# Kernel optimization log

Hardware: AMD Instinct MI355X
Metric: run time of the kernel (lower is better)

The kernel has to match this reference:

```python
import jax, jax.numpy as jnp
import numpy as np

N = 100_000      # nodes
E = 1_600_000    # edges
D = 128          # dim_in == dim_h
L = 3            # num_layers
G = 512          # num graphs in batch
EPS = 1e-5       # BatchNorm1d eps


def setup_inputs() -> dict:
    key = jax.random.key(0)
    k1, k2, k3, k4 = jax.random.split(key, 4)
    x = jax.random.normal(k1, (N, D), dtype=jnp.float32)
    edge_index = jax.random.randint(k2, (2, E), 0, N, dtype=jnp.int64)
    batch = jnp.sort(jax.random.randint(k3, (N,), 0, G, dtype=jnp.int64))
    Ws = jax.random.normal(k4, (L, D, D), dtype=jnp.float32) * 0.05
    bs = jnp.zeros((L, D), dtype=jnp.float32)
    gammas = jnp.ones((L, D), dtype=jnp.float32)
    betas = jnp.zeros((L, D), dtype=jnp.float32)
    return {"x": x, "edge_index": edge_index, "batch": batch,
            "Ws": Ws, "bs": bs, "gammas": gammas, "betas": betas}


def reference(x, edge_index, batch, Ws, bs, gammas, betas):
    src, dst = edge_index[0], edge_index[1]
    # GCN symmetric normalization with self-loops (PyG GCNConv default):
    # deg counts incoming edges at dst, +1 for the self-loop.
    deg = jnp.zeros((N,), dtype=x.dtype).at[dst].add(1.0) + 1.0
    inv_sqrt = jax.lax.rsqrt(deg)
    edge_coeff = inv_sqrt[src] * inv_sqrt[dst]   # [E]
    self_coeff = inv_sqrt * inv_sqrt             # [N] self-loop weight deg^-1

    h = x
    for i in range(L):
        hw = h @ Ws[i]                                           # [N, D]
        agg = (jnp.zeros_like(hw).at[dst].add(hw[src] * edge_coeff[:, None])
               + hw * self_coeff[:, None] + bs[i])               # [N, D]
        # BatchNorm1d (training-mode batch statistics, biased variance)
        mean = agg.mean(axis=0)
        var = agg.var(axis=0)
        hn = (agg - mean) * jax.lax.rsqrt(var + EPS) * gammas[i] + betas[i]
        h = jax.nn.relu(hn)

    # global_add_pool: scatter-add node features by graph id
    return jax.ops.segment_sum(h, batch, num_segments=G)        # [G, D]
```

## Files before the change

kernel.cpp:

```cpp
#include <hip/hip_runtime.h>

#define D 128
#define CHUNK 512
#define NSLICE 8
#define SLW 16

using short8 = __attribute__((ext_vector_type(8))) short;
using f32x4  = __attribute__((ext_vector_type(4))) float;
using f32x2  = __attribute__((ext_vector_type(2))) float;

__device__ __forceinline__ unsigned short f2bf(float f){
  unsigned u = __builtin_bit_cast(unsigned, f);
  u += 0x7fffu + ((u >> 16) & 1u);
  return (unsigned short)(u >> 16);
}
__device__ __forceinline__ float bflo2f(unsigned v){
  return __builtin_bit_cast(float, v << 16);
}
__device__ __forceinline__ float bfhi2f(unsigned v){
  return __builtin_bit_cast(float, v & 0xffff0000u);
}
__device__ __forceinline__ float bfs2f(unsigned short v){
  return __builtin_bit_cast(float, ((unsigned)v) << 16);
}
__device__ __forceinline__ unsigned cvtpk(float lo, float hi){
  unsigned r;
  asm("v_cvt_pk_bf16_f32 %0, %1, %2" : "=v"(r) : "v"(lo), "v"(hi));
  return r;
}

__global__ void k_deg(const int* __restrict__ dst, int* __restrict__ deg, int E){
  int e = blockIdx.x * 256 + threadIdx.x;
  if (e < E) atomicAdd(&deg[dst[e]], 1);
}

__global__ void k_chunksum(const int* __restrict__ deg, int* __restrict__ csum, int n){
  __shared__ int s[256];
  int tid = threadIdx.x;
  int n0 = blockIdx.x * CHUNK + tid * 2;
  int v = 0;
  if (n0     < n) v += deg[n0];
  if (n0 + 1 < n) v += deg[n0 + 1];
  s[tid] = v; __syncthreads();
  for (int off = 128; off > 0; off >>= 1){
    if (tid < off) s[tid] += s[tid + off];
    __syncthreads();
  }
  if (tid == 0) csum[blockIdx.x] = s[0];
}

__global__ void k_scanchunks(int* __restrict__ csum, int nchunks){
  __shared__ int s[256];
  int tid = threadIdx.x;
  int v = (tid < nchunks) ? csum[tid] : 0;
  s[tid] = v; __syncthreads();
  for (int off = 1; off < 256; off <<= 1){
    int t = (tid >= off) ? s[tid - off] : 0;
    __syncthreads();
    s[tid] += t;
    __syncthreads();
  }
  if (tid < nchunks) csum[tid] = s[tid] - v;
}

__global__ void k_offsets(const int* __restrict__ deg, const int* __restrict__ csum,
                          int* __restrict__ offs, float* __restrict__ inv, int n){
  __shared__ int s[256];
  int tid = threadIdx.x;
  int n0 = blockIdx.x * CHUNK + tid * 2;
  int d0 = (n0     < n) ? deg[n0]     : 0;
  int d1 = (n0 + 1 < n) ? deg[n0 + 1] : 0;
  int pair = d0 + d1;
  s[tid] = pair; __syncthreads();
  for (int off = 1; off < 256; off <<= 1){
    int t = (tid >= off) ? s[tid - off] : 0;
    __syncthreads();
    s[tid] += t;
    __syncthreads();
  }
  int excl = s[tid] - pair + csum[blockIdx.x];
  if (n0     <= n) offs[n0]     = excl;
  if (n0 + 1 <= n) offs[n0 + 1] = excl + d0;
  if (n0     < n) inv[n0]     = rsqrtf((float)(d0 + 1));
  if (n0 + 1 < n) inv[n0 + 1] = rsqrtf((float)(d1 + 1));
}

__global__ __launch_bounds__(256)
void k_csrfill(const int* __restrict__ src, const int* __restrict__ dst,
               const int* __restrict__ offs, int* __restrict__ cursor,
               int* __restrict__ csrc, int E, int n){
  int part = blockIdx.x & 7;
  int blk  = blockIdx.x >> 3;
  int nblk = gridDim.x >> 3;
  int per = (n + 7) / 8;
  int d0 = part * per, d1 = min(d0 + per, n);
  int stride = nblk * 256;
  for (int e = blk * 256 + threadIdx.x; e < E; e += stride){
    int d = dst[e];
    if (d >= d0 && d < d1){
      int s = src[e];
      int pos = offs[d] + atomicAdd(&cursor[d], 1);
      csrc[pos] = s;
    }
  }
}

#define WSTRIDE 136
__global__ __launch_bounds__(512)
void k_gemm(const float* __restrict__ hf, const unsigned short* __restrict__ hb,
            const float* __restrict__ W, const float* __restrict__ inv,
            const float* __restrict__ scale, const float* __restrict__ shift,
            int do_norm, unsigned short* __restrict__ hwS, int nrows){
  __shared__ unsigned short Wt[128 * WSTRIDE];
  int tid = threadIdx.x;
  for (int i = tid; i < 128 * 128; i += 512){
    int k = i >> 7, c = i & 127;
    Wt[c * WSTRIDE + k] = f2bf(W[i]);
  }
  __syncthreads();

  int wave = tid >> 6, lane = tid & 63;
  int r0 = blockIdx.x * 128 + wave * 16;
  int row = r0 + (lane & 15);
  int kg = lane >> 4;
  int rowc = row < nrows ? row : nrows - 1;

  short8 a[4];
  if (do_norm){
#pragma unroll
    for (int kt = 0; kt < 4; ++kt){
      int k0 = kt * 32 + kg * 8;
      int sl = k0 >> 4, o = k0 & 15;
      short8 raw = *(const short8*)(hb + ((long)sl * nrows + rowc) * SLW + o);
      unsigned u[4];
#pragma unroll
      for (int j = 0; j < 4; ++j){
        float lo = bfs2f((unsigned short)raw[2*j]);
        float hi = bfs2f((unsigned short)raw[2*j+1]);
        lo = fmaxf(0.f, lo * scale[k0+2*j]   + shift[k0+2*j]);
        hi = fmaxf(0.f, hi * scale[k0+2*j+1] + shift[k0+2*j+1]);
        u[j] = cvtpk(lo, hi);
      }
      a[kt] = *(short8*)u;
    }
  } else {
    const float* hrow = hf + (long)rowc * D;
#pragma unroll
    for (int kt = 0; kt < 4; ++kt){
      int k0 = kt * 32 + kg * 8;
      f32x4 v0 = *(const f32x4*)(hrow + k0);
      f32x4 v1 = *(const f32x4*)(hrow + k0 + 4);
      unsigned u[4];
      u[0] = cvtpk(v0[0], v0[1]);
      u[1] = cvtpk(v0[2], v0[3]);
      u[2] = cvtpk(v1[0], v1[1]);
      u[3] = cvtpk(v1[2], v1[3]);
      a[kt] = *(short8*)u;
    }
  }

  f32x4 acc[8] = {};
#pragma unroll
  for (int ct = 0; ct < 8; ++ct){
    int col = ct * 16 + (lane & 15);
    const unsigned short* bp = &Wt[col * WSTRIDE + kg * 8];
#pragma unroll
    for (int kt = 0; kt < 4; ++kt){
      short8 b = *(const short8*)(bp + kt * 32);
      acc[ct] = __builtin_amdgcn_mfma_f32_16x16x32_bf16(a[kt], b, acc[ct], 0, 0, 0);
    }
  }

  int colbase = lane & 15;
  int rowo = r0 + kg * 4;
  float ivr[4];
#pragma unroll
  for (int r = 0; r < 4; ++r) ivr[r] = inv[min(rowo + r, nrows - 1)];
#pragma unroll
  for (int ct = 0; ct < 8; ++ct){
#pragma unroll
    for (int r = 0; r < 4; ++r){
      int rr = rowo + r;
      if (rr < nrows)
        hwS[((long)ct * nrows + rr) * SLW + colbase] = f2bf(acc[ct][r] * ivr[r]);
    }
  }
}

__global__ __launch_bounds__(256)
void k_agg(const unsigned short* __restrict__ hwS, const float* __restrict__ inv,
           const int* __restrict__ offs, const int* __restrict__ csrc,
           const float* __restrict__ bias,
           unsigned* __restrict__ aggS, float* __restrict__ stats, int n,
           int ngroups){
  int g   = blockIdx.x & 7;
  int grp = blockIdx.x >> 3;
  int tid = threadIdx.x, lane = tid & 63, wv = tid >> 6;
  int ns = lane >> 3;
  int cp = lane & 7;
  int nwaves = ngroups * 4;
  int gw = grp * 4 + wv;
  int per = (n + nwaves - 1) / nwaves;
  int n0 = min(gw * per, n), n1 = min(n0 + per, n);

  const unsigned* slice = (const unsigned*)hwS + (long)g * n * 8;
  unsigned* oslice = aggS + (long)g * n * 8;

  float b0 = bias[g * 16 + cp * 2], b1 = bias[g * 16 + cp * 2 + 1];
  float s0 = 0, s1 = 0, q0 = 0, q1 = 0;

  for (int base = n0; base < n1; base += 8){
    int node = base + ns;
    bool act = node < n1;
    int ndc = act ? node : n1 - 1;
    int e  = offs[ndc];
    int ee = offs[ndc + 1];
    float a0 = 0, a1 = 0;

    int i0 = csrc[(e     < ee) ? e     : 0];
    int i1 = csrc[(e + 1 < ee) ? e + 1 : 0];
    int i2 = csrc[(e + 2 < ee) ? e + 2 : 0];
    int i3 = csrc[(e + 3 < ee) ? e + 3 : 0];
    while (__any(e < ee)){
      int j0 = csrc[(e + 4 < ee) ? e + 4 : 0];
      int j1 = csrc[(e + 5 < ee) ? e + 5 : 0];
      int j2 = csrc[(e + 6 < ee) ? e + 6 : 0];
      int j3 = csrc[(e + 7 < ee) ? e + 7 : 0];
      unsigned v0 = slice[i0 * 8 + cp];
      unsigned v1 = slice[i1 * 8 + cp];
      unsigned v2 = slice[i2 * 8 + cp];
      unsigned v3 = slice[i3 * 8 + cp];
      v0 = (e     < ee) ? v0 : 0u;
      v1 = (e + 1 < ee) ? v1 : 0u;
      v2 = (e + 2 < ee) ? v2 : 0u;
      v3 = (e + 3 < ee) ? v3 : 0u;
      a0 += (bflo2f(v0) + bflo2f(v1)) + (bflo2f(v2) + bflo2f(v3));
      a1 += (bfhi2f(v0) + bfhi2f(v1)) + (bfhi2f(v2) + bfhi2f(v3));
      i0 = j0; i1 = j1; i2 = j2; i3 = j3;
      e += 4;
    }

    if (act){
      unsigned selfv = slice[node * 8 + cp];
      float ivd = inv[node];
      a0 = (a0 + bflo2f(selfv)) * ivd + b0;
      a1 = (a1 + bfhi2f(selfv)) * ivd + b1;
      unsigned pk = ((unsigned)f2bf(a1) << 16) | (unsigned)f2bf(a0);
      __builtin_nontemporal_store(pk, oslice + node * 8 + cp);
      s0 += a0; s1 += a1; q0 += a0 * a0; q1 += a1 * a1;
    }
  }

  s0 += __shfl_xor(s0, 8, 64);  s1 += __shfl_xor(s1, 8, 64);
  q0 += __shfl_xor(q0, 8, 64);  q1 += __shfl_xor(q1, 8, 64);
  s0 += __shfl_xor(s0, 16, 64); s1 += __shfl_xor(s1, 16, 64);
  q0 += __shfl_xor(q0, 16, 64); q1 += __shfl_xor(q1, 16, 64);
  s0 += __shfl_xor(s0, 32, 64); s1 += __shfl_xor(s1, 32, 64);
  q0 += __shfl_xor(q0, 32, 64); q1 += __shfl_xor(q1, 32, 64);

  __shared__ float red[4][8][4];
  if (ns == 0){
    red[wv][cp][0] = s0; red[wv][cp][1] = s1;
    red[wv][cp][2] = q0; red[wv][cp][3] = q1;
  }
  __syncthreads();
  if (tid < 8){
    float t0 = 0, t1 = 0, t2 = 0, t3 = 0;
#pragma unroll
    for (int w = 0; w < 4; ++w){
      t0 += red[w][tid][0]; t1 += red[w][tid][1];
      t2 += red[w][tid][2]; t3 += red[w][tid][3];
    }
    int c = g * 16 + tid * 2;
    atomicAdd(&stats[c],           t0);
    atomicAdd(&stats[c + 1],       t1);
    atomicAdd(&stats[128 + c],     t2);
    atomicAdd(&stats[128 + c + 1], t3);
  }
}

__global__ void k_bn(const float* __restrict__ stats, const float* __restrict__ gamma,
                     const float* __restrict__ beta, float* __restrict__ scale,
                     float* __restrict__ shift, float invn){
  int c = threadIdx.x;
  float mean = stats[c] * invn;
  float var = stats[128 + c] * invn - mean * mean;
  float isd = rsqrtf(var + 1e-5f);
  float sc = gamma[c] * isd;
  scale[c] = sc;
  shift[c] = beta[c] - mean * sc;
}

__global__ __launch_bounds__(256)
void k_pool(const unsigned* __restrict__ aggS, const float* __restrict__ scale,
            const float* __restrict__ shift, const int* __restrict__ batch,
            float* __restrict__ out, int n){
  int tid = threadIdx.x, lane = tid & 63, wv = tid >> 6;
  int gw = blockIdx.x * 4 + wv;
  int n0 = gw * 64;
  if (n0 >= n) return;
  int n1 = min(n0 + 64, n);
  int c0 = lane * 2;
  int sl = lane >> 3, cp = lane & 7;
  long sbase = (long)sl * n * 8;
  float sc0 = scale[c0], sc1 = scale[c0 + 1];
  float sh0 = shift[c0], sh1 = shift[c0 + 1];
  int g = batch[n0];
  float a0 = 0, a1 = 0;
  for (int nd = n0; nd < n1; ++nd){
    int gn = batch[nd];
    if (gn != g){
      atomicAdd(&out[(long)g * D + c0],     a0);
      atomicAdd(&out[(long)g * D + c0 + 1], a1);
      a0 = 0; a1 = 0; g = gn;
    }
    unsigned v = aggS[sbase + (long)nd * 8 + cp];
    a0 += fmaxf(0.f, bflo2f(v) * sc0 + sh0);
    a1 += fmaxf(0.f, bfhi2f(v) * sc1 + sh1);
  }
  atomicAdd(&out[(long)g * D + c0],     a0);
  atomicAdd(&out[(long)g * D + c0 + 1], a1);
}

extern "C" void kernel_launch(void* const* d_in, const int* in_sizes, int n_in,
                              void* d_out, int out_size, void* d_ws, size_t ws_size,
                              hipStream_t stream){
  const float* x      = (const float*)d_in[0];
  const int*   ei     = (const int*)d_in[1];
  const int*   batch  = (const int*)d_in[2];
  const float* Ws     = (const float*)d_in[3];
  const float* bs     = (const float*)d_in[4];
  const float* gammas = (const float*)d_in[5];
  const float* betas  = (const float*)d_in[6];

  const int E_ = in_sizes[1] / 2;
  const int N_ = in_sizes[2];
  const int* src = ei;
  const int* dst = ei + E_;

  char* p = (char*)d_ws;
  auto alloc = [&](size_t bytes) -> void* {
    void* r = (void*)p;
    p += (bytes + 255) & ~(size_t)255;
    return r;
  };
  unsigned*       bufA   = (unsigned*)      alloc((size_t)N_ * D * 2);
  unsigned short* hwS    = (unsigned short*)alloc((size_t)N_ * D * 2);
  int*            deg    = (int*)           alloc((size_t)N_ * 4);
  float*          inv    = (float*)         alloc((size_t)N_ * 4);
  int*            offs   = (int*)           alloc((size_t)(N_ + 1) * 4);
  int*            cursor = (int*)           alloc((size_t)N_ * 4);
  int*            csrc   = (int*)           alloc((size_t)E_ * 4);
  float*          stats  = (float*)         alloc(3 * 256 * 4);
  float*          scales = (float*)         alloc(3 * 128 * 4);
  float*          shifts = (float*)         alloc(3 * 128 * 4);
  int*            csum   = (int*)           alloc(256 * 4);

  hipMemsetAsync(deg,    0, (size_t)N_ * 4, stream);
  hipMemsetAsync(cursor, 0, (size_t)N_ * 4, stream);
  hipMemsetAsync(stats,  0, 3 * 256 * 4, stream);
  hipMemsetAsync(d_out,  0, (size_t)out_size * 4, stream);

  int nchunks = (N_ + CHUNK - 1) / CHUNK;
  k_deg       <<<(E_ + 255) / 256, 256, 0, stream>>>(dst, deg, E_);
  k_chunksum  <<<nchunks, 256, 0, stream>>>(deg, csum, N_);
  k_scanchunks<<<1, 256, 0, stream>>>(csum, nchunks);
  k_offsets   <<<nchunks, 256, 0, stream>>>(deg, csum, offs, inv, N_);
  k_csrfill   <<<2048, 256, 0, stream>>>(src, dst, offs, cursor, csrc, E_, N_);

  int gemm_blocks = (N_ + 127) / 128;
  int ngroups = 256;
  for (int l = 0; l < 3; ++l){
    const float* sc = (l == 0) ? nullptr : scales + (l - 1) * 128;
    const float* sh = (l == 0) ? nullptr : shifts + (l - 1) * 128;
    k_gemm<<<gemm_blocks, 512, 0, stream>>>(x, (const unsigned short*)bufA,
                                            Ws + (size_t)l * D * D, inv, sc, sh,
                                            (l == 0) ? 0 : 1, hwS, N_);
    k_agg<<<ngroups * 8, 256, 0, stream>>>(hwS, inv, offs, csrc, bs + (size_t)l * D,
                                           bufA, stats + (size_t)l * 256, N_, ngroups);
    k_bn<<<1, 128, 0, stream>>>(stats + (size_t)l * 256, gammas + (size_t)l * D,
                                betas + (size_t)l * D, scales + (size_t)l * 128,
                                shifts + (size_t)l * 128, 1.0f / (float)N_);
  }
  k_pool<<<(N_ + 255) / 256, 256, 0, stream>>>(bufA, scales + 2 * 128, shifts + 2 * 128,
                                               batch, (float*)d_out, N_);
}
```

Before: 558.0 us.

## Sort nodes by degree within 64-node windows to balance aggregation waves

Adds a bitonic sort kernel that orders each 64-node window by in-degree, producing a permutation. The aggregation kernel then gives each wave one window, processed as 8 groups of 8 similar-degree nodes, so lanes in a group finish their edge loops together instead of waiting on the slowest node. This also replaces the old launch of 256 groups with one wave per window, creating many more blocks. It costs one extra small sort kernel, an indirect perm load per node, less contiguous output writes, and the nontemporal store is dropped.

```diff
diff --git a/kernel.cpp b/kernel.cpp
--- a/kernel.cpp
+++ b/kernel.cpp
@@ -105,6 +105,30 @@
   }
 }
 
+__global__ __launch_bounds__(256)
+void k_sortwin(const int* __restrict__ deg, int* __restrict__ perm, int n, int W){
+  int wv = threadIdx.x >> 6, lane = threadIdx.x & 63;
+  int win = blockIdx.x * 4 + wv;
+  if (win >= W) return;
+  int idx = win * 64 + lane;
+  int nd2 = idx;
+  int dg  = (idx < n) ? deg[idx] : 0x7fffffff;
+#pragma unroll
+  for (int k = 2; k <= 64; k <<= 1){
+#pragma unroll
+    for (int j = k >> 1; j > 0; j >>= 1){
+      int odg = __shfl_xor(dg, j, 64);
+      int ond = __shfl_xor(nd2, j, 64);
+      bool dir = (lane & k) != 0;
+      bool smaller = (odg < dg) || (odg == dg && ond < nd2);
+      bool lower = (lane & j) == 0;
+      bool take = (lower ^ dir) ? smaller : !smaller;
+      if (take){ dg = odg; nd2 = ond; }
+    }
+  }
+  perm[win * 64 + lane] = (nd2 < n) ? nd2 : -1;
+}
+
 #define WSTRIDE 136
 __global__ __launch_bounds__(512)
 void k_gemm(const float* __restrict__ hf, const unsigned short* __restrict__ hb,
@@ -190,18 +214,13 @@
 __global__ __launch_bounds__(256)
 void k_agg(const unsigned short* __restrict__ hwS, const float* __restrict__ inv,
            const int* __restrict__ offs, const int* __restrict__ csrc,
-           const float* __restrict__ bias,
-           unsigned* __restrict__ aggS, float* __restrict__ stats, int n,
-           int ngroups){
+           const int* __restrict__ perm, const float* __restrict__ bias,
+           unsigned* __restrict__ aggS, float* __restrict__ stats, int n, int W){
   int g   = blockIdx.x & 7;
-  int grp = blockIdx.x >> 3;
   int tid = threadIdx.x, lane = tid & 63, wv = tid >> 6;
+  int win = (blockIdx.x >> 3) * 4 + wv;
   int ns = lane >> 3;
   int cp = lane & 7;
-  int nwaves = ngroups * 4;
-  int gw = grp * 4 + wv;
-  int per = (n + nwaves - 1) / nwaves;
-  int n0 = min(gw * per, n), n1 = min(n0 + per, n);
 
   const unsigned* slice = (const unsigned*)hwS + (long)g * n * 8;
   unsigned* oslice = aggS + (long)g * n * 8;
@@ -209,45 +228,49 @@
   float b0 = bias[g * 16 + cp * 2], b1 = bias[g * 16 + cp * 2 + 1];
   float s0 = 0, s1 = 0, q0 = 0, q1 = 0;
 
-  for (int base = n0; base < n1; base += 8){
-    int node = base + ns;
-    bool act = node < n1;
-    int ndc = act ? node : n1 - 1;
-    int e  = offs[ndc];
-    int ee = offs[ndc + 1];
-    float a0 = 0, a1 = 0;
-
-    int i0 = csrc[(e     < ee) ? e     : 0];
-    int i1 = csrc[(e + 1 < ee) ? e + 1 : 0];
-    int i2 = csrc[(e + 2 < ee) ? e + 2 : 0];
-    int i3 = csrc[(e + 3 < ee) ? e + 3 : 0];
-    while (__any(e < ee)){
-      int j0 = csrc[(e + 4 < ee) ? e + 4 : 0];
-      int j1 = csrc[(e + 5 < ee) ? e + 5 : 0];
-      int j2 = csrc[(e + 6 < ee) ? e + 6 : 0];
-      int j3 = csrc[(e + 7 < ee) ? e + 7 : 0];
-      unsigned v0 = slice[i0 * 8 + cp];
-      unsigned v1 = slice[i1 * 8 + cp];
-      unsigned v2 = slice[i2 * 8 + cp];
-      unsigned v3 = slice[i3 * 8 + cp];
-      v0 = (e     < ee) ? v0 : 0u;
-      v1 = (e + 1 < ee) ? v1 : 0u;
-      v2 = (e + 2 < ee) ? v2 : 0u;
-      v3 = (e + 3 < ee) ? v3 : 0u;
-      a0 += (bflo2f(v0) + bflo2f(v1)) + (bflo2f(v2) + bflo2f(v3));
-      a1 += (bfhi2f(v0) + bfhi2f(v1)) + (bfhi2f(v2) + bfhi2f(v3));
-      i0 = j0; i1 = j1; i2 = j2; i3 = j3;
-      e += 4;
-    }
-
-    if (act){
-      unsigned selfv = slice[node * 8 + cp];
-      float ivd = inv[node];
-      a0 = (a0 + bflo2f(selfv)) * ivd + b0;
-      a1 = (a1 + bfhi2f(selfv)) * ivd + b1;
-      unsigned pk = ((unsigned)f2bf(a1) << 16) | (unsigned)f2bf(a0);
-      __builtin_nontemporal_store(pk, oslice + node * 8 + cp);
-      s0 += a0; s1 += a1; q0 += a0 * a0; q1 += a1 * a1;
+  if (win < W){
+#pragma unroll 1
+    for (int c = 0; c < 8; ++c){
+      int node = perm[win * 64 + c * 8 + ns];
+      bool act = node >= 0;
+      int ndc = act ? node : 0;
+      int e  = offs[ndc];
+      int ee = act ? offs[ndc + 1] : e;
+      int eemax = max(ee - 1, 0);
+      float a0 = 0, a1 = 0;
+
+      int i0 = csrc[min(e,     eemax)];
+      int i1 = csrc[min(e + 1, eemax)];
+      int i2 = csrc[min(e + 2, eemax)];
+      int i3 = csrc[min(e + 3, eemax)];
+      while (__any(e < ee)){
+        int j0 = csrc[min(e + 4, eemax)];
+        int j1 = csrc[min(e + 5, eemax)];
+        int j2 = csrc[min(e + 6, eemax)];
+        int j3 = csrc[min(e + 7, eemax)];
+        unsigned v0 = slice[i0 * 8 + cp];
+        unsigned v1 = slice[i1 * 8 + cp];
+        unsigned v2 = slice[i2 * 8 + cp];
+        unsigned v3 = slice[i3 * 8 + cp];
+        v0 = (e     < ee) ? v0 : 0u;
+        v1 = (e + 1 < ee) ? v1 : 0u;
+        v2 = (e + 2 < ee) ? v2 : 0u;
+        v3 = (e + 3 < ee) ? v3 : 0u;
+        a0 += (bflo2f(v0) + bflo2f(v1)) + (bflo2f(v2) + bflo2f(v3));
+        a1 += (bfhi2f(v0) + bfhi2f(v1)) + (bfhi2f(v2) + bfhi2f(v3));
+        i0 = j0; i1 = j1; i2 = j2; i3 = j3;
+        e += 4;
+      }
+
+      if (act){
+        unsigned selfv = slice[node * 8 + cp];
+        float ivd = inv[node];
+        a0 = (a0 + bflo2f(selfv)) * ivd + b0;
+        a1 = (a1 + bfhi2f(selfv)) * ivd + b1;
+        unsigned pk = ((unsigned)f2bf(a1) << 16) | (unsigned)f2bf(a0);
+        oslice[node * 8 + cp] = pk;
+        s0 += a0; s1 += a1; q0 += a0 * a0; q1 += a1 * a1;
+      }
     }
   }
 
@@ -344,6 +367,7 @@
     p += (bytes + 255) & ~(size_t)255;
     return r;
   };
+  const int W = (N_ + 63) / 64;
   unsigned*       bufA   = (unsigned*)      alloc((size_t)N_ * D * 2);
   unsigned short* hwS    = (unsigned short*)alloc((size_t)N_ * D * 2);
   int*            deg    = (int*)           alloc((size_t)N_ * 4);
@@ -351,6 +375,7 @@
   int*            offs   = (int*)           alloc((size_t)(N_ + 1) * 4);
   int*            cursor = (int*)           alloc((size_t)N_ * 4);
   int*            csrc   = (int*)           alloc((size_t)E_ * 4);
+  int*            perm   = (int*)           alloc((size_t)W * 64 * 4);
   float*          stats  = (float*)         alloc(3 * 256 * 4);
   float*          scales = (float*)         alloc(3 * 128 * 4);
   float*          shifts = (float*)         alloc(3 * 128 * 4);
@@ -367,17 +392,19 @@
   k_scanchunks<<<1, 256, 0, stream>>>(csum, nchunks);
   k_offsets   <<<nchunks, 256, 0, stream>>>(deg, csum, offs, inv, N_);
   k_csrfill   <<<2048, 256, 0, stream>>>(src, dst, offs, cursor, csrc, E_, N_);
+  k_sortwin   <<<(W + 3) / 4, 256, 0, stream>>>(deg, perm, N_, W);
 
   int gemm_blocks = (N_ + 127) / 128;
-  int ngroups = 256;
+  int agg_blocks = ((W + 3) / 4) * 8;
   for (int l = 0; l < 3; ++l){
     const float* sc = (l == 0) ? nullptr : scales + (l - 1) * 128;
     const float* sh = (l == 0) ? nullptr : shifts + (l - 1) * 128;
     k_gemm<<<gemm_blocks, 512, 0, stream>>>(x, (const unsigned short*)bufA,
                                             Ws + (size_t)l * D * D, inv, sc, sh,
                                             (l == 0) ? 0 : 1, hwS, N_);
-    k_agg<<<ngroups * 8, 256, 0, stream>>>(hwS, inv, offs, csrc, bs + (size_t)l * D,
-                                           bufA, stats + (size_t)l * 256, N_, ngroups);
+    k_agg<<<agg_blocks, 256, 0, stream>>>(hwS, inv, offs, csrc, perm,
+                                          bs + (size_t)l * D,
+                                          bufA, stats + (size_t)l * 256, N_, W);
     k_bn<<<1, 128, 0, stream>>>(stats + (size_t)l * 256, gammas + (size_t)l * D,
                                 betas + (size_t)l * D, scales + (size_t)l * 128,
                                 shifts + (size_t)l * 128, 1.0f / (float)N_);
```

Result: slower. 601.2 us (+7.8%).
